# Optimization experiments

Measured on AMD Instinct MI355X. Metric: run time of the kernel, lower is better.

## Reference

```python
import jax, jax.numpy as jnp
import numpy as np

B, H, P, L = 8, 512, 512, 2048
HIGH_STAB, LOW_STAB = 0.9, 0.99  # 0 <= high < |lambda| <= low <= 1 (discrete dynamics)


def setup_inputs() -> dict:
    key = jax.random.key(0)
    k_u, k_mag, k_ph, k_b, k_c, k_d = jax.random.split(key, 6)
    u = jax.random.normal(k_u, (B, H, L), dtype=jnp.float32)
    # Frozen diagonal reservoir state matrix Lambda_bar: complex eigenvalues with
    # magnitude in (high_stability, low_stability], random phase (stored as real/imag pairs).
    mag = jax.random.uniform(k_mag, (P,), minval=HIGH_STAB, maxval=LOW_STAB)
    phase = jax.random.uniform(k_ph, (P,), minval=0.0, maxval=2.0 * np.pi)
    Lambda_bar_ri = jnp.stack([mag * jnp.cos(phase), mag * jnp.sin(phase)], axis=-1)  # (P,2)
    B_bar_ri = jax.random.normal(k_b, (P, H, 2), dtype=jnp.float32)  # complex B_bar as real pairs
    C_ri = jax.random.normal(k_c, (H, P, 2), dtype=jnp.float32)      # complex C as real pairs
    D = jax.random.normal(k_d, (H, H), dtype=jnp.float32)
    return {"u": u, "Lambda_bar_ri": Lambda_bar_ri, "B_bar_ri": B_bar_ri, "C_ri": C_ri, "D": D}


def _binary_op(e_i, e_j):
    A_i, Bu_i = e_i
    A_j, Bu_j = e_j
    return (A_j * A_i, A_j * Bu_i + Bu_j)


def reference(u, Lambda_bar_ri, B_bar_ri, C_ri, D):
    Lam = jax.lax.complex(Lambda_bar_ri[:, 0], Lambda_bar_ri[:, 1])        # (P,)
    B_bar = jax.lax.complex(B_bar_ri[..., 0], B_bar_ri[..., 1])            # (P,H)
    C = jax.lax.complex(C_ri[..., 0], C_ri[..., 1])                        # (H,P)
    # Bu_t = B_bar @ u_t for all t, batched: (B,P,L) complex
    Bu = jnp.einsum('ph,bhl->bpl', B_bar, u.astype(B_bar.dtype))
    A = jnp.broadcast_to(Lam[None, :, None], Bu.shape)                     # (B,P,L)
    # Parallel associative scan: x_t = Lam * x_{t-1} + Bu_t
    _, x = jax.lax.associative_scan(_binary_op, (A, Bu), axis=2)           # (B,P,L)
    C_A_Bu = jnp.einsum('hp,bpl->bhl', C, x).real                          # (B,H,L)
    # torch.einsum('hh,bhl->bhl', D, u) uses only the diagonal of D
    Du = jnp.diagonal(D)[None, :, None] * u
    return jax.nn.gelu(C_A_Bu + Du, approximate=False)
```

## Files before the change

### kernel.cpp

```cpp
#include <hip/hip_runtime.h>
#include <cstdint>
#include <cstddef>

#define BB 8
#define HH 512
#define PP 512
#define LL 2048

typedef __attribute__((ext_vector_type(8))) __bf16 bf16x8;
typedef __attribute__((ext_vector_type(4))) float f32x4;

__device__ __forceinline__ uint16_t f2bf(float f) {
  uint32_t u = __builtin_bit_cast(uint32_t, f);
  u += 0x7FFFu + ((u >> 16) & 1u);
  return (uint16_t)(u >> 16);
}

__device__ __forceinline__ void async_copy16(const void* gptr, void* ldsptr) {
  __builtin_amdgcn_global_load_lds(
      (const __attribute__((address_space(1))) unsigned int*)gptr,
      (__attribute__((address_space(3))) unsigned int*)ldsptr,
      16, 0, 0);
}

__global__ __launch_bounds__(256) void prep_mats(
    const float* __restrict__ Bbar, const float* __restrict__ Cri,
    const float* __restrict__ Dm,
    uint16_t* __restrict__ A1, uint16_t* __restrict__ A2,
    float* __restrict__ Dd) {
  int idx = blockIdx.x * 256 + threadIdx.x;
  int p = idx >> 9, h = idx & 511;
  A1[(size_t)p * 512 + h]          = f2bf(Bbar[((size_t)p * 512 + h) * 2 + 0]);
  A1[(size_t)(512 + p) * 512 + h]  = f2bf(Bbar[((size_t)p * 512 + h) * 2 + 1]);
  int h2 = idx >> 9, p2 = idx & 511;
  A2[(size_t)h2 * 1024 + p2]        = f2bf( Cri[((size_t)h2 * 512 + p2) * 2 + 0]);
  A2[(size_t)h2 * 1024 + 512 + p2]  = f2bf(-Cri[((size_t)h2 * 512 + p2) * 2 + 1]);
  if (idx < 512) Dd[idx] = Dm[(size_t)idx * 512 + idx];
}

__global__ __launch_bounds__(256) void scan_kernel(
    const float* __restrict__ Lam, uint16_t* __restrict__ Bu) {
  const int gt = blockIdx.x * 256 + threadIdx.x;
  const int wave = gt >> 6, lane = gt & 63;
  const int b = wave >> 9, p = wave & 511;
  const float lr = Lam[p * 2 + 0], li = Lam[p * 2 + 1];
  float ar = lr, ai = li;
#pragma unroll
  for (int s = 0; s < 5; ++s) { float nr = ar * ar - ai * ai, ni = 2.f * ar * ai; ar = nr; ai = ni; }

  uint16_t* rowre = Bu + ((size_t)(b * 1024 + p)) * 2048 + lane * 32;
  uint16_t* rowim = Bu + ((size_t)(b * 1024 + 512 + p)) * 2048 + lane * 32;
  uint4 vr[4], vi[4];
#pragma unroll
  for (int q = 0; q < 4; ++q) { vr[q] = ((const uint4*)rowre)[q]; vi[q] = ((const uint4*)rowim)[q]; }

  float xr[32], xi[32];
  float sr = 0.f, si = 0.f;
#pragma unroll
  for (int q = 0; q < 4; ++q) {
    uint32_t wr[4] = {vr[q].x, vr[q].y, vr[q].z, vr[q].w};
    uint32_t wi[4] = {vi[q].x, vi[q].y, vi[q].z, vi[q].w};
#pragma unroll
    for (int d = 0; d < 4; ++d) {
      float br0 = __builtin_bit_cast(float, wr[d] << 16);
      float bi0 = __builtin_bit_cast(float, wi[d] << 16);
      float br1 = __builtin_bit_cast(float, wr[d] & 0xFFFF0000u);
      float bi1 = __builtin_bit_cast(float, wi[d] & 0xFFFF0000u);
      int j = q * 8 + d * 2;
      float nr = lr * sr - li * si + br0, ni = lr * si + li * sr + bi0;
      sr = nr; si = ni; xr[j] = sr; xi[j] = si;
      nr = lr * sr - li * si + br1; ni = lr * si + li * sr + bi1;
      sr = nr; si = ni; xr[j + 1] = sr; xi[j + 1] = si;
    }
  }
  float Ar = ar, Ai = ai, Sr = sr, Si = si;
#pragma unroll
  for (int off = 1; off < 64; off <<= 1) {
    float pAr = __shfl_up(Ar, off), pAi = __shfl_up(Ai, off);
    float pSr = __shfl_up(Sr, off), pSi = __shfl_up(Si, off);
    if (lane >= off) {
      float tSr = Ar * pSr - Ai * pSi + Sr;
      float tSi = Ar * pSi + Ai * pSr + Si;
      float tAr = Ar * pAr - Ai * pAi;
      float tAi = Ar * pAi + Ai * pAr;
      Sr = tSr; Si = tSi; Ar = tAr; Ai = tAi;
    }
  }
  float Cr = __shfl_up(Sr, 1), Ci = __shfl_up(Si, 1);
  if (lane == 0) { Cr = 0.f; Ci = 0.f; }
  float fr_ = lr * Cr - li * Ci, fi_ = lr * Ci + li * Cr;
#pragma unroll
  for (int j = 0; j < 32; ++j) {
    xr[j] += fr_; xi[j] += fi_;
    float nfr = fr_ * lr - fi_ * li, nfi = fr_ * li + fi_ * lr;
    fr_ = nfr; fi_ = nfi;
  }
#pragma unroll
  for (int q = 0; q < 4; ++q) {
    uint32_t wr[4], wi[4];
#pragma unroll
    for (int d = 0; d < 4; ++d) {
      int j = q * 8 + d * 2;
      wr[d] = (uint32_t)f2bf(xr[j]) | ((uint32_t)f2bf(xr[j + 1]) << 16);
      wi[d] = (uint32_t)f2bf(xi[j]) | ((uint32_t)f2bf(xi[j + 1]) << 16);
    }
    ((uint4*)rowre)[q] = make_uint4(wr[0], wr[1], wr[2], wr[3]);
    ((uint4*)rowim)[q] = make_uint4(wi[0], wi[1], wi[2], wi[3]);
  }
}

__global__ __launch_bounds__(256) void gemm1_fused(
    const uint16_t* __restrict__ A, const float* __restrict__ U,
    uint16_t* __restrict__ Bu) {
  __shared__ __align__(16) uint16_t Alds[128 * 32];
  __shared__ __align__(16) uint16_t Blds[128 * 40];
  const int t = threadIdx.x, lane = t & 63, w = t >> 6;
  const int m0 = blockIdx.y * 128, n0 = blockIdx.x * 128, b = blockIdx.z;

  const int ra = t >> 2;
  const int qa = ((t & 3) ^ ((ra >> 1) & 3)) * 8;
  const uint16_t* gA0 = A + (size_t)(m0 + ra) * 512 + qa;
  const uint16_t* gA1 = A + (size_t)(m0 + 64 + ra) * 512 + qa;

  const int kp = t >> 4, lg = t & 15;
  const float* gB = U + ((size_t)b * 512 + 2 * kp) * 2048 + n0 + lg * 8;
  const int bcol = ((kp >> 2) ^ (lg & 3)) * 8 + (kp & 3) * 2;

  f32x4 acc[4][4];
#pragma unroll
  for (int i = 0; i < 4; ++i)
#pragma unroll
    for (int j = 0; j < 4; ++j) acc[i][j] = (f32x4){0.f, 0.f, 0.f, 0.f};

  const int wm = (w >> 1) * 64, wn = (w & 1) * 64;
  const int fr = lane & 15, fq = lane >> 4;
  const int aswz = (fq ^ ((fr >> 1) & 3)) * 8;

  for (int kb = 0; kb < 512; kb += 32) {
    async_copy16(gA0 + kb, Alds + (size_t)t * 8);
    async_copy16(gA1 + kb, Alds + 2048 + (size_t)t * 8);
    const float* s0 = gB + (size_t)kb * 2048;
    float4 a0 = *(const float4*)(s0);
    float4 a1 = *(const float4*)(s0 + 4);
    float4 b0 = *(const float4*)(s0 + 2048);
    float4 b1 = *(const float4*)(s0 + 2052);
    float r0[8] = {a0.x, a0.y, a0.z, a0.w, a1.x, a1.y, a1.z, a1.w};
    float r1[8] = {b0.x, b0.y, b0.z, b0.w, b1.x, b1.y, b1.z, b1.w};
#pragma unroll
    for (int j = 0; j < 8; ++j) {
      uint32_t wv = (uint32_t)f2bf(r0[j]) | ((uint32_t)f2bf(r1[j]) << 16);
      *(uint32_t*)&Blds[(lg * 8 + j) * 40 + bcol] = wv;
    }
    __syncthreads();
    bf16x8 af[4], bfr[4];
#pragma unroll
    for (int i = 0; i < 4; ++i)
      af[i] = *(const bf16x8*)&Alds[(wm + i * 16 + fr) * 32 + aswz];
#pragma unroll
    for (int j = 0; j < 4; ++j) {
      int n = wn + j * 16 + fr;
      bfr[j] = *(const bf16x8*)&Blds[n * 40 + ((fq ^ ((n >> 3) & 3)) * 8)];
    }
#pragma unroll
    for (int i = 0; i < 4; ++i)
#pragma unroll
      for (int j = 0; j < 4; ++j)
        acc[i][j] = __builtin_amdgcn_mfma_f32_16x16x32_bf16(af[i], bfr[j], acc[i][j], 0, 0, 0);
    __syncthreads();
  }

  uint16_t* O = Bu + ((size_t)b * 1024 + m0) * 2048 + n0;
#pragma unroll
  for (int i = 0; i < 4; ++i)
#pragma unroll
    for (int j = 0; j < 4; ++j)
#pragma unroll
      for (int r = 0; r < 4; ++r) {
        int mm = wm + i * 16 + fq * 4 + r;
        int nn = wn + j * 16 + fr;
        O[(size_t)mm * 2048 + nn] = f2bf(acc[i][j][r]);
      }
}

__global__ __launch_bounds__(256) void gemm2_fused(
    const uint16_t* __restrict__ A, const uint16_t* __restrict__ X,
    float* __restrict__ Out, const float* __restrict__ Dd,
    const float* __restrict__ Uu) {
  __shared__ __align__(16) uint16_t Alds[128 * 32];
  __shared__ __align__(16) uint16_t Blds[128 * 40];
  const int t = threadIdx.x, lane = t & 63, w = t >> 6;
  const int m0 = blockIdx.y * 128, n0 = blockIdx.x * 128, b = blockIdx.z;

  const int ra = t >> 2;
  const int qa = ((t & 3) ^ ((ra >> 1) & 3)) * 8;
  const uint16_t* gA0 = A + (size_t)(m0 + ra) * 1024 + qa;
  const uint16_t* gA1 = A + (size_t)(m0 + 64 + ra) * 1024 + qa;

  const int kp = t >> 4, lg = t & 15;
  const uint16_t* gB = X + ((size_t)b * 1024 + 2 * kp) * 2048 + n0 + lg * 8;
  const int bcol = ((kp >> 2) ^ (lg & 3)) * 8 + (kp & 3) * 2;

  f32x4 acc[4][4];
#pragma unroll
  for (int i = 0; i < 4; ++i)
#pragma unroll
    for (int j = 0; j < 4; ++j) acc[i][j] = (f32x4){0.f, 0.f, 0.f, 0.f};

  const int wm = (w >> 1) * 64, wn = (w & 1) * 64;
  const int fr = lane & 15, fq = lane >> 4;
  const int aswz = (fq ^ ((fr >> 1) & 3)) * 8;

  for (int kb = 0; kb < 1024; kb += 32) {
    async_copy16(gA0 + kb, Alds + (size_t)t * 8);
    async_copy16(gA1 + kb, Alds + 2048 + (size_t)t * 8);
    const uint16_t* s0 = gB + (size_t)kb * 2048;
    uint4 q0 = *(const uint4*)(s0);
    uint4 q1 = *(const uint4*)(s0 + 2048);
    uint32_t u0[4] = {q0.x, q0.y, q0.z, q0.w};
    uint32_t u1[4] = {q1.x, q1.y, q1.z, q1.w};
#pragma unroll
    for (int d = 0; d < 4; ++d) {
      uint32_t lo = (u0[d] & 0xFFFFu) | (u1[d] << 16);
      uint32_t hi = (u0[d] >> 16) | (u1[d] & 0xFFFF0000u);
      *(uint32_t*)&Blds[(lg * 8 + 2 * d + 0) * 40 + bcol] = lo;
      *(uint32_t*)&Blds[(lg * 8 + 2 * d + 1) * 40 + bcol] = hi;
    }
    __syncthreads();
    bf16x8 af[4], bfr[4];
#pragma unroll
    for (int i = 0; i < 4; ++i)
      af[i] = *(const bf16x8*)&Alds[(wm + i * 16 + fr) * 32 + aswz];
#pragma unroll
    for (int j = 0; j < 4; ++j) {
      int n = wn + j * 16 + fr;
      bfr[j] = *(const bf16x8*)&Blds[n * 40 + ((fq ^ ((n >> 3) & 3)) * 8)];
    }
#pragma unroll
    for (int i = 0; i < 4; ++i)
#pragma unroll
      for (int j = 0; j < 4; ++j)
        acc[i][j] = __builtin_amdgcn_mfma_f32_16x16x32_bf16(af[i], bfr[j], acc[i][j], 0, 0, 0);
    __syncthreads();
  }

  const size_t base = ((size_t)b * 512 + m0) * 2048 + n0;
  float* O = Out + base;
  const float* Ub = Uu + base;
#pragma unroll
  for (int i = 0; i < 4; ++i)
#pragma unroll
    for (int r = 0; r < 4; ++r) {
      int mm = wm + i * 16 + fq * 4 + r;
      float dv = Dd[m0 + mm];
#pragma unroll
      for (int j = 0; j < 4; ++j) {
        int nn = wn + j * 16 + fr;
        float xv = acc[i][j][r] + dv * Ub[(size_t)mm * 2048 + nn];
        O[(size_t)mm * 2048 + nn] = 0.5f * xv * (1.f + erff(xv * 0.70710678118654752f));
      }
    }
}

extern "C" void kernel_launch(void* const* d_in, const int* in_sizes, int n_in,
                              void* d_out, int out_size, void* d_ws, size_t ws_size,
                              hipStream_t stream) {
  const float* u    = (const float*)d_in[0];
  const float* Lam  = (const float*)d_in[1];
  const float* Bbar = (const float*)d_in[2];
  const float* Cri  = (const float*)d_in[3];
  const float* Dm   = (const float*)d_in[4];
  float* out = (float*)d_out;

  char* ws = (char*)d_ws;
  uint16_t* Bu = (uint16_t*)(ws);
  uint16_t* A1 = (uint16_t*)(ws + 33554432);
  uint16_t* A2 = (uint16_t*)(ws + 34603008);
  float*    Dd = (float*)   (ws + 35651584);

  prep_mats<<<1024, 256, 0, stream>>>(Bbar, Cri, Dm, A1, A2, Dd);
  gemm1_fused<<<dim3(16, 8, BB), 256, 0, stream>>>(A1, u, Bu);
  scan_kernel<<<1024, 256, 0, stream>>>(Lam, Bu);
  gemm2_fused<<<dim3(16, 4, BB), 256, 0, stream>>>(A2, Bu, out, Dd, u);
}
```

Baseline: 199.8 us.

## Double-buffer LDS tiles in both GEMM kernels to overlap loads with MFMA

Both GEMM kernels now keep two LDS buffers for the A and B tiles. The next k-slice is prefetched (async copies for A, register loads for B) while MFMAs run on the current buffer, which leaves one barrier per iteration instead of two. This is meant to hide global memory latency behind compute. In exchange it doubles LDS use per block, which may lower occupancy, and adds register pressure from the prefetched B values.

```diff
diff --git a/kernel.cpp b/kernel.cpp
--- a/kernel.cpp
+++ b/kernel.cpp
@@ -112,8 +112,8 @@
 __global__ __launch_bounds__(256) void gemm1_fused(
     const uint16_t* __restrict__ A, const float* __restrict__ U,
     uint16_t* __restrict__ Bu) {
-  __shared__ __align__(16) uint16_t Alds[128 * 32];
-  __shared__ __align__(16) uint16_t Blds[128 * 40];
+  __shared__ __align__(16) uint16_t Alds[2][128 * 32];
+  __shared__ __align__(16) uint16_t Blds[2][128 * 40];
   const int t = threadIdx.x, lane = t & 63, w = t >> 6;
   const int m0 = blockIdx.y * 128, n0 = blockIdx.x * 128, b = blockIdx.z;
 
@@ -136,37 +136,60 @@
   const int fr = lane & 15, fq = lane >> 4;
   const int aswz = (fq ^ ((fr >> 1) & 3)) * 8;
 
-  for (int kb = 0; kb < 512; kb += 32) {
-    async_copy16(gA0 + kb, Alds + (size_t)t * 8);
-    async_copy16(gA1 + kb, Alds + 2048 + (size_t)t * 8);
-    const float* s0 = gB + (size_t)kb * 2048;
-    float4 a0 = *(const float4*)(s0);
-    float4 a1 = *(const float4*)(s0 + 4);
-    float4 b0 = *(const float4*)(s0 + 2048);
-    float4 b1 = *(const float4*)(s0 + 2052);
-    float r0[8] = {a0.x, a0.y, a0.z, a0.w, a1.x, a1.y, a1.z, a1.w};
-    float r1[8] = {b0.x, b0.y, b0.z, b0.w, b1.x, b1.y, b1.z, b1.w};
-#pragma unroll
-    for (int j = 0; j < 8; ++j) {
-      uint32_t wv = (uint32_t)f2bf(r0[j]) | ((uint32_t)f2bf(r1[j]) << 16);
-      *(uint32_t*)&Blds[(lg * 8 + j) * 40 + bcol] = wv;
-    }
-    __syncthreads();
+  float4 pb0, pb1, pb2, pb3;
+  async_copy16(gA0, &Alds[0][t * 8]);
+  async_copy16(gA1, &Alds[0][2048 + t * 8]);
+  pb0 = *(const float4*)(gB);
+  pb1 = *(const float4*)(gB + 4);
+  pb2 = *(const float4*)(gB + 2048);
+  pb3 = *(const float4*)(gB + 2052);
+  {
+    float r0[8] = {pb0.x, pb0.y, pb0.z, pb0.w, pb1.x, pb1.y, pb1.z, pb1.w};
+    float r1[8] = {pb2.x, pb2.y, pb2.z, pb2.w, pb3.x, pb3.y, pb3.z, pb3.w};
+#pragma unroll
+    for (int j = 0; j < 8; ++j)
+      *(uint32_t*)&Blds[0][(lg * 8 + j) * 40 + bcol] =
+          (uint32_t)f2bf(r0[j]) | ((uint32_t)f2bf(r1[j]) << 16);
+  }
+  __syncthreads();
+
+#pragma unroll 2
+  for (int it = 0; it < 16; ++it) {
+    const int cur = it & 1, nxt = cur ^ 1;
+    const bool pre = (it < 15);
+    if (pre) {
+      const int kb = (it + 1) * 32;
+      async_copy16(gA0 + kb, &Alds[nxt][t * 8]);
+      async_copy16(gA1 + kb, &Alds[nxt][2048 + t * 8]);
+      const float* s0 = gB + (size_t)kb * 2048;
+      pb0 = *(const float4*)(s0);
+      pb1 = *(const float4*)(s0 + 4);
+      pb2 = *(const float4*)(s0 + 2048);
+      pb3 = *(const float4*)(s0 + 2052);
+    }
     bf16x8 af[4], bfr[4];
 #pragma unroll
     for (int i = 0; i < 4; ++i)
-      af[i] = *(const bf16x8*)&Alds[(wm + i * 16 + fr) * 32 + aswz];
+      af[i] = *(const bf16x8*)&Alds[cur][(wm + i * 16 + fr) * 32 + aswz];
 #pragma unroll
     for (int j = 0; j < 4; ++j) {
       int n = wn + j * 16 + fr;
-      bfr[j] = *(const bf16x8*)&Blds[n * 40 + ((fq ^ ((n >> 3) & 3)) * 8)];
+      bfr[j] = *(const bf16x8*)&Blds[cur][n * 40 + ((fq ^ ((n >> 3) & 3)) * 8)];
     }
 #pragma unroll
     for (int i = 0; i < 4; ++i)
 #pragma unroll
       for (int j = 0; j < 4; ++j)
         acc[i][j] = __builtin_amdgcn_mfma_f32_16x16x32_bf16(af[i], bfr[j], acc[i][j], 0, 0, 0);
-    __syncthreads();
+    if (pre) {
+      float r0[8] = {pb0.x, pb0.y, pb0.z, pb0.w, pb1.x, pb1.y, pb1.z, pb1.w};
+      float r1[8] = {pb2.x, pb2.y, pb2.z, pb2.w, pb3.x, pb3.y, pb3.z, pb3.w};
+#pragma unroll
+      for (int j = 0; j < 8; ++j)
+        *(uint32_t*)&Blds[nxt][(lg * 8 + j) * 40 + bcol] =
+            (uint32_t)f2bf(r0[j]) | ((uint32_t)f2bf(r1[j]) << 16);
+      __syncthreads();
+    }
   }
 
   uint16_t* O = Bu + ((size_t)b * 1024 + m0) * 2048 + n0;
@@ -186,8 +209,8 @@
     const uint16_t* __restrict__ A, const uint16_t* __restrict__ X,
     float* __restrict__ Out, const float* __restrict__ Dd,
     const float* __restrict__ Uu) {
-  __shared__ __align__(16) uint16_t Alds[128 * 32];
-  __shared__ __align__(16) uint16_t Blds[128 * 40];
+  __shared__ __align__(16) uint16_t Alds[2][128 * 32];
+  __shared__ __align__(16) uint16_t Blds[2][128 * 40];
   const int t = threadIdx.x, lane = t & 63, w = t >> 6;
   const int m0 = blockIdx.y * 128, n0 = blockIdx.x * 128, b = blockIdx.z;
 
@@ -210,37 +233,58 @@
   const int fr = lane & 15, fq = lane >> 4;
   const int aswz = (fq ^ ((fr >> 1) & 3)) * 8;
 
-  for (int kb = 0; kb < 1024; kb += 32) {
-    async_copy16(gA0 + kb, Alds + (size_t)t * 8);
-    async_copy16(gA1 + kb, Alds + 2048 + (size_t)t * 8);
-    const uint16_t* s0 = gB + (size_t)kb * 2048;
-    uint4 q0 = *(const uint4*)(s0);
-    uint4 q1 = *(const uint4*)(s0 + 2048);
+  uint4 q0, q1;
+  async_copy16(gA0, &Alds[0][t * 8]);
+  async_copy16(gA1, &Alds[0][2048 + t * 8]);
+  q0 = *(const uint4*)(gB);
+  q1 = *(const uint4*)(gB + 2048);
+  {
     uint32_t u0[4] = {q0.x, q0.y, q0.z, q0.w};
     uint32_t u1[4] = {q1.x, q1.y, q1.z, q1.w};
 #pragma unroll
     for (int d = 0; d < 4; ++d) {
-      uint32_t lo = (u0[d] & 0xFFFFu) | (u1[d] << 16);
-      uint32_t hi = (u0[d] >> 16) | (u1[d] & 0xFFFF0000u);
-      *(uint32_t*)&Blds[(lg * 8 + 2 * d + 0) * 40 + bcol] = lo;
-      *(uint32_t*)&Blds[(lg * 8 + 2 * d + 1) * 40 + bcol] = hi;
-    }
-    __syncthreads();
+      *(uint32_t*)&Blds[0][(lg * 8 + 2 * d + 0) * 40 + bcol] = (u0[d] & 0xFFFFu) | (u1[d] << 16);
+      *(uint32_t*)&Blds[0][(lg * 8 + 2 * d + 1) * 40 + bcol] = (u0[d] >> 16) | (u1[d] & 0xFFFF0000u);
+    }
+  }
+  __syncthreads();
+
+#pragma unroll 2
+  for (int it = 0; it < 32; ++it) {
+    const int cur = it & 1, nxt = cur ^ 1;
+    const bool pre = (it < 31);
+    if (pre) {
+      const int kb = (it + 1) * 32;
+      async_copy16(gA0 + kb, &Alds[nxt][t * 8]);
+      async_copy16(gA1 + kb, &Alds[nxt][2048 + t * 8]);
+      const uint16_t* s0 = gB + (size_t)kb * 2048;
+      q0 = *(const uint4*)(s0);
+      q1 = *(const uint4*)(s0 + 2048);
+    }
     bf16x8 af[4], bfr[4];
 #pragma unroll
     for (int i = 0; i < 4; ++i)
-      af[i] = *(const bf16x8*)&Alds[(wm + i * 16 + fr) * 32 + aswz];
+      af[i] = *(const bf16x8*)&Alds[cur][(wm + i * 16 + fr) * 32 + aswz];
 #pragma unroll
     for (int j = 0; j < 4; ++j) {
       int n = wn + j * 16 + fr;
-      bfr[j] = *(const bf16x8*)&Blds[n * 40 + ((fq ^ ((n >> 3) & 3)) * 8)];
+      bfr[j] = *(const bf16x8*)&Blds[cur][n * 40 + ((fq ^ ((n >> 3) & 3)) * 8)];
     }
 #pragma unroll
     for (int i = 0; i < 4; ++i)
 #pragma unroll
       for (int j = 0; j < 4; ++j)
         acc[i][j] = __builtin_amdgcn_mfma_f32_16x16x32_bf16(af[i], bfr[j], acc[i][j], 0, 0, 0);
-    __syncthreads();
+    if (pre) {
+      uint32_t u0[4] = {q0.x, q0.y, q0.z, q0.w};
+      uint32_t u1[4] = {q1.x, q1.y, q1.z, q1.w};
+#pragma unroll
+      for (int d = 0; d < 4; ++d) {
+        *(uint32_t*)&Blds[nxt][(lg * 8 + 2 * d + 0) * 40 + bcol] = (u0[d] & 0xFFFFu) | (u1[d] << 16);
+        *(uint32_t*)&Blds[nxt][(lg * 8 + 2 * d + 1) * 40 + bcol] = (u0[d] >> 16) | (u1[d] & 0xFFFF0000u);
+      }
+      __syncthreads();
+    }
   }
 
   const size_t base = ((size_t)b * 512 + m0) * 2048 + n0;
```

After: 193.0 us. 3.4% less time.

## Restructure GEMMs: direct-register A fragments, double-buffered B tiles, taller blocks

Applied to the files above, without the earlier changes.

Both GEMMs now use 512-thread blocks covering 512 rows by 64 columns. Each wave loads its A-operand fragments straight from global memory into registers, prefetched one k-step ahead, so A no longer goes through LDS. The B tile is double-buffered in LDS with 128-deep k chunks and a single barrier per chunk, which cuts synchronisation and lets global loads overlap the MFMA work. The cost is that A fragments are re-read from global memory or L2 by every block, and there are fewer blocks in the grid (512 and 256).

```diff
diff --git a/kernel.cpp b/kernel.cpp
--- a/kernel.cpp
+++ b/kernel.cpp
@@ -14,13 +14,6 @@
   uint32_t u = __builtin_bit_cast(uint32_t, f);
   u += 0x7FFFu + ((u >> 16) & 1u);
   return (uint16_t)(u >> 16);
-}
-
-__device__ __forceinline__ void async_copy16(const void* gptr, void* ldsptr) {
-  __builtin_amdgcn_global_load_lds(
-      (const __attribute__((address_space(1))) unsigned int*)gptr,
-      (__attribute__((address_space(3))) unsigned int*)ldsptr,
-      16, 0, 0);
 }
 
 __global__ __launch_bounds__(256) void prep_mats(
@@ -109,22 +102,19 @@
   }
 }
 
-__global__ __launch_bounds__(256) void gemm1_fused(
+__global__ __launch_bounds__(512) void gemm1_fused(
     const uint16_t* __restrict__ A, const float* __restrict__ U,
     uint16_t* __restrict__ Bu) {
-  __shared__ __align__(16) uint16_t Alds[128 * 32];
-  __shared__ __align__(16) uint16_t Blds[128 * 40];
+  __shared__ __align__(16) uint16_t Blds[2][64 * 136];
   const int t = threadIdx.x, lane = t & 63, w = t >> 6;
-  const int m0 = blockIdx.y * 128, n0 = blockIdx.x * 128, b = blockIdx.z;
-
-  const int ra = t >> 2;
-  const int qa = ((t & 3) ^ ((ra >> 1) & 3)) * 8;
-  const uint16_t* gA0 = A + (size_t)(m0 + ra) * 512 + qa;
-  const uint16_t* gA1 = A + (size_t)(m0 + 64 + ra) * 512 + qa;
-
-  const int kp = t >> 4, lg = t & 15;
-  const float* gB = U + ((size_t)b * 512 + 2 * kp) * 2048 + n0 + lg * 8;
-  const int bcol = ((kp >> 2) ^ (lg & 3)) * 8 + (kp & 3) * 2;
+  const int m0 = blockIdx.y * 512, n0 = blockIdx.x * 64, b = blockIdx.z;
+  const int fr = lane & 15, fq = lane >> 4;
+
+  const int kr = t >> 3, lc = t & 7;
+  const int wcol = (((kr >> 2) ^ lc) << 3) + (kr & 3) * 2;
+  const float* gB = U + ((size_t)b * 512 + 2 * kr) * 2048 + n0 + lc * 8;
+
+  const uint16_t* gA = A + (size_t)(m0 + w * 64 + fr) * 512 + fq * 8;
 
   f32x4 acc[4][4];
 #pragma unroll
@@ -132,73 +122,90 @@
 #pragma unroll
     for (int j = 0; j < 4; ++j) acc[i][j] = (f32x4){0.f, 0.f, 0.f, 0.f};
 
-  const int wm = (w >> 1) * 64, wn = (w & 1) * 64;
-  const int fr = lane & 15, fq = lane >> 4;
-  const int aswz = (fq ^ ((fr >> 1) & 3)) * 8;
-
-  for (int kb = 0; kb < 512; kb += 32) {
-    async_copy16(gA0 + kb, Alds + (size_t)t * 8);
-    async_copy16(gA1 + kb, Alds + 2048 + (size_t)t * 8);
-    const float* s0 = gB + (size_t)kb * 2048;
-    float4 a0 = *(const float4*)(s0);
-    float4 a1 = *(const float4*)(s0 + 4);
-    float4 b0 = *(const float4*)(s0 + 2048);
-    float4 b1 = *(const float4*)(s0 + 2052);
-    float r0[8] = {a0.x, a0.y, a0.z, a0.w, a1.x, a1.y, a1.z, a1.w};
-    float r1[8] = {b0.x, b0.y, b0.z, b0.w, b1.x, b1.y, b1.z, b1.w};
-#pragma unroll
-    for (int j = 0; j < 8; ++j) {
-      uint32_t wv = (uint32_t)f2bf(r0[j]) | ((uint32_t)f2bf(r1[j]) << 16);
-      *(uint32_t*)&Blds[(lg * 8 + j) * 40 + bcol] = wv;
-    }
-    __syncthreads();
-    bf16x8 af[4], bfr[4];
-#pragma unroll
-    for (int i = 0; i < 4; ++i)
-      af[i] = *(const bf16x8*)&Alds[(wm + i * 16 + fr) * 32 + aswz];
-#pragma unroll
-    for (int j = 0; j < 4; ++j) {
-      int n = wn + j * 16 + fr;
-      bfr[j] = *(const bf16x8*)&Blds[n * 40 + ((fq ^ ((n >> 3) & 3)) * 8)];
-    }
-#pragma unroll
-    for (int i = 0; i < 4; ++i)
+  int rb[4], hj[4];
+#pragma unroll
+  for (int j = 0; j < 4; ++j) { int n = j * 16 + fr; rb[j] = n * 136; hj[j] = n >> 3; }
+
+  float4 p0, p1, p2, p3;
+  p0 = *(const float4*)(gB);
+  p1 = *(const float4*)(gB + 4);
+  p2 = *(const float4*)(gB + 2048);
+  p3 = *(const float4*)(gB + 2052);
+  {
+    float r0[8] = {p0.x, p0.y, p0.z, p0.w, p1.x, p1.y, p1.z, p1.w};
+    float r1[8] = {p2.x, p2.y, p2.z, p2.w, p3.x, p3.y, p3.z, p3.w};
+#pragma unroll
+    for (int j = 0; j < 8; ++j)
+      *(uint32_t*)&Blds[0][(lc * 8 + j) * 136 + wcol] =
+          (uint32_t)f2bf(r0[j]) | ((uint32_t)f2bf(r1[j]) << 16);
+  }
+  bf16x8 afr[2][4];
+#pragma unroll
+  for (int i = 0; i < 4; ++i) afr[0][i] = *(const bf16x8*)(gA + i * 8192);
+  __syncthreads();
+
+  for (int p = 0; p < 4; ++p) {
+    const int cb = p & 1;
+    if (p < 3) {
+      const float* sp = gB + (size_t)((p + 1) * 128) * 2048;
+      p0 = *(const float4*)(sp);
+      p1 = *(const float4*)(sp + 4);
+      p2 = *(const float4*)(sp + 2048);
+      p3 = *(const float4*)(sp + 2052);
+    }
+#pragma unroll
+    for (int s = 0; s < 4; ++s) {
+      if (p < 3 || s < 3) {
+        const int ks = p * 128 + (s + 1) * 32;
+#pragma unroll
+        for (int i = 0; i < 4; ++i)
+          afr[(s + 1) & 1][i] = *(const bf16x8*)(gA + i * 8192 + ks);
+      }
+      bf16x8 bfr[4];
 #pragma unroll
       for (int j = 0; j < 4; ++j)
-        acc[i][j] = __builtin_amdgcn_mfma_f32_16x16x32_bf16(af[i], bfr[j], acc[i][j], 0, 0, 0);
-    __syncthreads();
-  }
-
-  uint16_t* O = Bu + ((size_t)b * 1024 + m0) * 2048 + n0;
+        bfr[j] = *(const bf16x8*)&Blds[cb][rb[j] + ((((s * 4 + fq) ^ hj[j])) << 3)];
+#pragma unroll
+      for (int i = 0; i < 4; ++i)
+#pragma unroll
+        for (int j = 0; j < 4; ++j)
+          acc[i][j] = __builtin_amdgcn_mfma_f32_16x16x32_bf16(afr[s & 1][i], bfr[j], acc[i][j], 0, 0, 0);
+    }
+    if (p < 3) {
+      float r0[8] = {p0.x, p0.y, p0.z, p0.w, p1.x, p1.y, p1.z, p1.w};
+      float r1[8] = {p2.x, p2.y, p2.z, p2.w, p3.x, p3.y, p3.z, p3.w};
+#pragma unroll
+      for (int j = 0; j < 8; ++j)
+        *(uint32_t*)&Blds[cb ^ 1][(lc * 8 + j) * 136 + wcol] =
+            (uint32_t)f2bf(r0[j]) | ((uint32_t)f2bf(r1[j]) << 16);
+      __syncthreads();
+    }
+  }
+
+  uint16_t* O = Bu + ((size_t)b * 1024 + m0 + w * 64) * 2048 + n0;
 #pragma unroll
   for (int i = 0; i < 4; ++i)
 #pragma unroll
     for (int j = 0; j < 4; ++j)
 #pragma unroll
-      for (int r = 0; r < 4; ++r) {
-        int mm = wm + i * 16 + fq * 4 + r;
-        int nn = wn + j * 16 + fr;
-        O[(size_t)mm * 2048 + nn] = f2bf(acc[i][j][r]);
-      }
-}
-
-__global__ __launch_bounds__(256) void gemm2_fused(
+      for (int r = 0; r < 4; ++r)
+        O[(size_t)(i * 16 + fq * 4 + r) * 2048 + j * 16 + fr] = f2bf(acc[i][j][r]);
+}
+
+__global__ __launch_bounds__(512) void gemm2_fused(
     const uint16_t* __restrict__ A, const uint16_t* __restrict__ X,
     float* __restrict__ Out, const float* __restrict__ Dd,
     const float* __restrict__ Uu) {
-  __shared__ __align__(16) uint16_t Alds[128 * 32];
-  __shared__ __align__(16) uint16_t Blds[128 * 40];
+  __shared__ __align__(16) uint16_t Blds[2][64 * 136];
   const int t = threadIdx.x, lane = t & 63, w = t >> 6;
-  const int m0 = blockIdx.y * 128, n0 = blockIdx.x * 128, b = blockIdx.z;
-
-  const int ra = t >> 2;
-  const int qa = ((t & 3) ^ ((ra >> 1) & 3)) * 8;
-  const uint16_t* gA0 = A + (size_t)(m0 + ra) * 1024 + qa;
-  const uint16_t* gA1 = A + (size_t)(m0 + 64 + ra) * 1024 + qa;
-
-  const int kp = t >> 4, lg = t & 15;
-  const uint16_t* gB = X + ((size_t)b * 1024 + 2 * kp) * 2048 + n0 + lg * 8;
-  const int bcol = ((kp >> 2) ^ (lg & 3)) * 8 + (kp & 3) * 2;
+  const int n0 = blockIdx.x * 64, b = blockIdx.z;
+  const int fr = lane & 15, fq = lane >> 4;
+
+  const int kr = t >> 3, lc = t & 7;
+  const int wcol = (((kr >> 2) ^ lc) << 3) + (kr & 3) * 2;
+  const uint16_t* gB = X + ((size_t)b * 1024 + 2 * kr) * 2048 + n0 + lc * 8;
+
+  const uint16_t* gA = A + (size_t)(w * 64 + fr) * 1024 + fq * 8;
 
   f32x4 acc[4][4];
 #pragma unroll
@@ -206,55 +213,76 @@
 #pragma unroll
     for (int j = 0; j < 4; ++j) acc[i][j] = (f32x4){0.f, 0.f, 0.f, 0.f};
 
-  const int wm = (w >> 1) * 64, wn = (w & 1) * 64;
-  const int fr = lane & 15, fq = lane >> 4;
-  const int aswz = (fq ^ ((fr >> 1) & 3)) * 8;
-
-  for (int kb = 0; kb < 1024; kb += 32) {
-    async_copy16(gA0 + kb, Alds + (size_t)t * 8);
-    async_copy16(gA1 + kb, Alds + 2048 + (size_t)t * 8);
-    const uint16_t* s0 = gB + (size_t)kb * 2048;
-    uint4 q0 = *(const uint4*)(s0);
-    uint4 q1 = *(const uint4*)(s0 + 2048);
+  int rb[4], hj[4];
+#pragma unroll
+  for (int j = 0; j < 4; ++j) { int n = j * 16 + fr; rb[j] = n * 136; hj[j] = n >> 3; }
+
+  uint4 q0, q1;
+  q0 = *(const uint4*)(gB);
+  q1 = *(const uint4*)(gB + 2048);
+  {
     uint32_t u0[4] = {q0.x, q0.y, q0.z, q0.w};
     uint32_t u1[4] = {q1.x, q1.y, q1.z, q1.w};
 #pragma unroll
     for (int d = 0; d < 4; ++d) {
-      uint32_t lo = (u0[d] & 0xFFFFu) | (u1[d] << 16);
-      uint32_t hi = (u0[d] >> 16) | (u1[d] & 0xFFFF0000u);
-      *(uint32_t*)&Blds[(lg * 8 + 2 * d + 0) * 40 + bcol] = lo;
-      *(uint32_t*)&Blds[(lg * 8 + 2 * d + 1) * 40 + bcol] = hi;
-    }
-    __syncthreads();
-    bf16x8 af[4], bfr[4];
-#pragma unroll
-    for (int i = 0; i < 4; ++i)
-      af[i] = *(const bf16x8*)&Alds[(wm + i * 16 + fr) * 32 + aswz];
-#pragma unroll
-    for (int j = 0; j < 4; ++j) {
-      int n = wn + j * 16 + fr;
-      bfr[j] = *(const bf16x8*)&Blds[n * 40 + ((fq ^ ((n >> 3) & 3)) * 8)];
-    }
-#pragma unroll
-    for (int i = 0; i < 4; ++i)
+      *(uint32_t*)&Blds[0][(lc * 8 + 2 * d + 0) * 136 + wcol] = (u0[d] & 0xFFFFu) | (u1[d] << 16);
+      *(uint32_t*)&Blds[0][(lc * 8 + 2 * d + 1) * 136 + wcol] = (u0[d] >> 16) | (u1[d] & 0xFFFF0000u);
+    }
+  }
+  bf16x8 afr[2][4];
+#pragma unroll
+  for (int i = 0; i < 4; ++i) afr[0][i] = *(const bf16x8*)(gA + i * 16384);
+  __syncthreads();
+
+  for (int p = 0; p < 8; ++p) {
+    const int cb = p & 1;
+    if (p < 7) {
+      const uint16_t* sp = gB + (size_t)((p + 1) * 128) * 2048;
+      q0 = *(const uint4*)(sp);
+      q1 = *(const uint4*)(sp + 2048);
+    }
+#pragma unroll
+    for (int s = 0; s < 4; ++s) {
+      if (p < 7 || s < 3) {
+        const int ks = p * 128 + (s + 1) * 32;
+#pragma unroll
+        for (int i = 0; i < 4; ++i)
+          afr[(s + 1) & 1][i] = *(const bf16x8*)(gA + i * 16384 + ks);
+      }
+      bf16x8 bfr[4];
 #pragma unroll
       for (int j = 0; j < 4; ++j)
-        acc[i][j] = __builtin_amdgcn_mfma_f32_16x16x32_bf16(af[i], bfr[j], acc[i][j], 0, 0, 0);
-    __syncthreads();
-  }
-
-  const size_t base = ((size_t)b * 512 + m0) * 2048 + n0;
+        bfr[j] = *(const bf16x8*)&Blds[cb][rb[j] + ((((s * 4 + fq) ^ hj[j])) << 3)];
+#pragma unroll
+      for (int i = 0; i < 4; ++i)
+#pragma unroll
+        for (int j = 0; j < 4; ++j)
+          acc[i][j] = __builtin_amdgcn_mfma_f32_16x16x32_bf16(afr[s & 1][i], bfr[j], acc[i][j], 0, 0, 0);
+    }
+    if (p < 7) {
+      uint32_t u0[4] = {q0.x, q0.y, q0.z, q0.w};
+      uint32_t u1[4] = {q1.x, q1.y, q1.z, q1.w};
+#pragma unroll
+      for (int d = 0; d < 4; ++d) {
+        *(uint32_t*)&Blds[cb ^ 1][(lc * 8 + 2 * d + 0) * 136 + wcol] = (u0[d] & 0xFFFFu) | (u1[d] << 16);
+        *(uint32_t*)&Blds[cb ^ 1][(lc * 8 + 2 * d + 1) * 136 + wcol] = (u0[d] >> 16) | (u1[d] & 0xFFFF0000u);
+      }
+      __syncthreads();
+    }
+  }
+
+  const size_t base = ((size_t)b * 512 + w * 64) * 2048 + n0;
   float* O = Out + base;
   const float* Ub = Uu + base;
 #pragma unroll
   for (int i = 0; i < 4; ++i)
 #pragma unroll
     for (int r = 0; r < 4; ++r) {
-      int mm = wm + i * 16 + fq * 4 + r;
-      float dv = Dd[m0 + mm];
+      int mm = i * 16 + fq * 4 + r;
+      float dv = Dd[w * 64 + mm];
 #pragma unroll
       for (int j = 0; j < 4; ++j) {
-        int nn = wn + j * 16 + fr;
+        int nn = j * 16 + fr;
         float xv = acc[i][j][r] + dv * Ub[(size_t)mm * 2048 + nn];
         O[(size_t)mm * 2048 + nn] = 0.5f * xv * (1.f + erff(xv * 0.70710678118654752f));
       }
@@ -278,7 +306,7 @@
   float*    Dd = (float*)   (ws + 35651584);
 
   prep_mats<<<1024, 256, 0, stream>>>(Bbar, Cri, Dm, A1, A2, Dd);
-  gemm1_fused<<<dim3(16, 8, BB), 256, 0, stream>>>(A1, u, Bu);
+  gemm1_fused<<<dim3(32, 2, BB), 512, 0, stream>>>(A1, u, Bu);
   scan_kernel<<<1024, 256, 0, stream>>>(Lam, Bu);
-  gemm2_fused<<<dim3(16, 4, BB), 256, 0, stream>>>(A2, Bu, out, Dd, u);
-}
+  gemm2_fused<<<dim3(32, 1, BB), 512, 0, stream>>>(A2, Bu, out, Dd, u);
+}
```

New measurement: 205.3 us. +2.8%, slower.
